# Performance work log

Hardware: AMD Instinct MI355X
Metric: run time of the kernel (lower is better)

Reference implementation:

```python
import jax, jax.numpy as jnp
import numpy as np

B, H, L, E = 32, 8, 512, 3
N_VARS = 8
TOP_P = 0.5
NOISE_EPS = 0.01
EPS = 1e-10


def setup_inputs() -> dict:
    key = jax.random.key(0)
    k1, k2, k3 = jax.random.split(key, 3)
    scale = 1.0 / np.sqrt(L)  # sane logits for softmax
    x = jax.random.normal(k1, (B, H, L, L), dtype=jnp.float32)
    gate_w = jax.random.normal(k2, (E, L), dtype=jnp.float32) * scale
    noise_w = jax.random.normal(k3, (E, L), dtype=jnp.float32) * scale
    return {"x": x, "gate_w": gate_w, "noise_w": noise_w}


def _build_masks(L, n_vars):
    # Vectorized version of the torch per-k loop building [L, 3, L] masks.
    N = L // n_vars
    j = jnp.arange(L)          # target position
    k = jnp.arange(L)[:, None]  # source position
    S = ((j % N == k % N) & (j != k)).astype(jnp.float32)   # same offset, different var
    T = ((j // N) == (k // N)).astype(jnp.float32)           # same variable block
    ST = 1.0 - S - T
    return jnp.stack([S, T, ST], axis=1)  # [L, 3, L]


def _noisy_top_p_gating(xf, gate_w, noise_w, key):
    # xf: [BH, L, L] -> logits [BH, L, E]
    clean_logits = jnp.einsum('ble,ne->bln', xf, gate_w)
    noise_stddev = jax.nn.softplus(jnp.einsum('ble,ne->bln', xf, noise_w)) + NOISE_EPS
    noisy_logits = clean_logits + jax.random.normal(key, clean_logits.shape, clean_logits.dtype) * noise_stddev
    probs = jax.nn.softmax(noisy_logits, axis=-1)  # softmax over experts (dim 2)
    # dynamic (entropy) loss: sum over L dim (dim=1), mean over rest
    loss_dynamic = -(probs * jnp.log(probs + EPS)).sum(axis=1).mean()
    # sort descending over experts
    order = jnp.argsort(-probs, axis=-1)
    sorted_probs = jnp.take_along_axis(probs, order, axis=-1)
    cum = jnp.cumsum(sorted_probs, axis=-1)
    mask = cum > TOP_P
    # keep the first expert that crosses the threshold
    thr_idx = jnp.argmax(mask.astype(jnp.int32), axis=-1)          # [BH, L]
    thr_mask = jnp.arange(E) == thr_idx[..., None]                 # one-hot bool
    mask = mask & ~thr_mask
    # scatter kept (mask==0) sorted positions back to original expert ids:
    # top_p_mask[..., sorted_indices[..., k]] = (mask[..., k] == 0)
    inv = jnp.argsort(order, axis=-1)
    top_p_mask = jnp.take_along_axis((~mask).astype(jnp.float32), inv, axis=-1)
    # importance loss on masked sorted probs summed over batch dim
    kept = jnp.where(mask, 0.0, sorted_probs)
    importance = kept.sum(axis=0)  # [L, E]
    loss_importance = jnp.var(importance, ddof=1) / (importance.mean() ** 2 + EPS)
    loss = loss_importance + 0.1 * loss_dynamic
    return top_p_mask, loss


def reference(x, gate_w, noise_w):
    Bx, Hx, Lx, _ = x.shape
    xf = x.reshape(Bx * Hx, Lx, Lx)
    gates, loss = _noisy_top_p_gating(xf, gate_w, noise_w, jax.random.key(42))
    gates = gates.reshape(Bx, Hx, Lx, E).astype(jnp.float32)
    masks = _build_masks(Lx, N_VARS)            # [L, 3, L]
    mask_base = jnp.eye(Lx, dtype=jnp.float32)[None, None]
    out = jnp.einsum('bhli,lid->bhld', gates, masks) + mask_base
    return (out, loss)
```

## Files before the change

kernel.cpp:

```cpp
#include <hip/hip_runtime.h>
#include <cstdint>
#include <cstddef>


namespace {

constexpr int kBH = 256;
constexpr int kL = 512;
constexpr int kE = 3;
constexpr int kRows = kBH * kL;

typedef float v4f __attribute__((ext_vector_type(4)));

__device__ __forceinline__ uint32_t rotl32(uint32_t v, int n) {
  return (v << n) | (v >> (32 - n));
}

__device__ __forceinline__ void threefry2x32_k42(uint32_t& x0, uint32_t& x1) {
  const uint32_t ks0 = 0u;
  const uint32_t ks1 = 42u;
  const uint32_t ks2 = 0u ^ 42u ^ 0x1BD11BDAu;
  x0 += ks0; x1 += ks1;
#define TF_ROUND(r) { x0 += x1; x1 = rotl32(x1, (r)); x1 ^= x0; }
  TF_ROUND(13) TF_ROUND(15) TF_ROUND(26) TF_ROUND(6)
  x0 += ks1; x1 += ks2 + 1u;
  TF_ROUND(17) TF_ROUND(29) TF_ROUND(16) TF_ROUND(24)
  x0 += ks2; x1 += ks0 + 2u;
  TF_ROUND(13) TF_ROUND(15) TF_ROUND(26) TF_ROUND(6)
  x0 += ks0; x1 += ks1 + 3u;
  TF_ROUND(17) TF_ROUND(29) TF_ROUND(16) TF_ROUND(24)
  x0 += ks1; x1 += ks2 + 4u;
  TF_ROUND(13) TF_ROUND(15) TF_ROUND(26) TF_ROUND(6)
  x0 += ks2; x1 += ks0 + 5u;
#undef TF_ROUND
}

__device__ __forceinline__ uint32_t jax_random_bits(uint32_t flat_idx) {
  uint32_t x0 = 0u;
  uint32_t x1 = flat_idx;
  threefry2x32_k42(x0, x1);
  return x0 ^ x1;
}

__device__ float bits_to_normal(uint32_t bits) {
#pragma clang fp contract(off)
  const uint32_t fb = (bits >> 9) | 0x3F800000u;
  const float f = __uint_as_float(fb) - 1.0f;
  const float lo = -0.99999994f;
  float u = f * 2.0f + lo;
  u = fmaxf(lo, u);
  float w = -log1pf(-(u * u));
  float p;
  if (w < 5.0f) {
    w = w - 2.5f;
    p = 2.81022636e-08f;
    p = 3.43273939e-07f + p * w;
    p = -3.5233877e-06f + p * w;
    p = -4.39150654e-06f + p * w;
    p = 0.00021858087f + p * w;
    p = -0.00125372503f + p * w;
    p = -0.00417768164f + p * w;
    p = 0.246640727f + p * w;
    p = 1.50140941f + p * w;
  } else {
    w = sqrtf(w) - 3.0f;
    p = -0.000200214257f;
    p = 0.000100950558f + p * w;
    p = 0.00134934322f + p * w;
    p = -0.00367342844f + p * w;
    p = 0.00573950773f + p * w;
    p = -0.0076224613f + p * w;
    p = 0.00943887047f + p * w;
    p = 1.00167406f + p * w;
    p = 2.83297682f + p * w;
  }
  const float einv = p * u;
  return 1.41421354f * einv;
}

__device__ __forceinline__ float softplus_f32(float v) {
#pragma clang fp contract(off)
  const float amax = fmaxf(v, 0.0f);
  return amax + log1pf(expf(-fabsf(v)));
}

#define LOADG(BUF, OFF)                                                     \
  _Pragma("unroll")                                                         \
  for (int i_ = 0; i_ < 4; ++i_)                                            \
    BUF[i_] = *reinterpret_cast<const float4*>(xr + (OFF) + i_ * 4);

#define COMP16(BUF, KB)                                                     \
  {                                                                         \
    _Pragma("unroll")                                                       \
    for (int j_ = 0; j_ < 4; ++j_) {                                        \
      const int k_ = (KB) + j_ * 4;                                         \
      const float4 wg0 = *reinterpret_cast<const float4*>(gw + k_);         \
      const float4 wg1 = *reinterpret_cast<const float4*>(gw + kL + k_);    \
      const float4 wg2 = *reinterpret_cast<const float4*>(gw + 2*kL + k_);  \
      const float4 wn0 = *reinterpret_cast<const float4*>(nw + k_);         \
      const float4 wn1 = *reinterpret_cast<const float4*>(nw + kL + k_);    \
      const float4 wn2 = *reinterpret_cast<const float4*>(nw + 2*kL + k_);  \
      const float4 xq = BUF[j_];                                            \
      accg[0] = fmaf(xq.x, wg0.x, accg[0]);                                 \
      accg[1] = fmaf(xq.x, wg1.x, accg[1]);                                 \
      accg[2] = fmaf(xq.x, wg2.x, accg[2]);                                 \
      accn[0] = fmaf(xq.x, wn0.x, accn[0]);                                 \
      accn[1] = fmaf(xq.x, wn1.x, accn[1]);                                 \
      accn[2] = fmaf(xq.x, wn2.x, accn[2]);                                 \
      accg[0] = fmaf(xq.y, wg0.y, accg[0]);                                 \
      accg[1] = fmaf(xq.y, wg1.y, accg[1]);                                 \
      accg[2] = fmaf(xq.y, wg2.y, accg[2]);                                 \
      accn[0] = fmaf(xq.y, wn0.y, accn[0]);                                 \
      accn[1] = fmaf(xq.y, wn1.y, accn[1]);                                 \
      accn[2] = fmaf(xq.y, wn2.y, accn[2]);                                 \
      accg[0] = fmaf(xq.z, wg0.z, accg[0]);                                 \
      accg[1] = fmaf(xq.z, wg1.z, accg[1]);                                 \
      accg[2] = fmaf(xq.z, wg2.z, accg[2]);                                 \
      accn[0] = fmaf(xq.z, wn0.z, accn[0]);                                 \
      accn[1] = fmaf(xq.z, wn1.z, accn[1]);                                 \
      accn[2] = fmaf(xq.z, wn2.z, accn[2]);                                 \
      accg[0] = fmaf(xq.w, wg0.w, accg[0]);                                 \
      accg[1] = fmaf(xq.w, wg1.w, accg[1]);                                 \
      accg[2] = fmaf(xq.w, wg2.w, accg[2]);                                 \
      accn[0] = fmaf(xq.w, wn0.w, accn[0]);                                 \
      accn[1] = fmaf(xq.w, wn1.w, accn[1]);                                 \
      accn[2] = fmaf(xq.w, wn2.w, accn[2]);                                 \
    }                                                                       \
  }

__global__ __launch_bounds__(256) void gating_kernel(
    const float* __restrict__ x, const float* __restrict__ gw,
    const float* __restrict__ nw, float* __restrict__ g_out,
    float* __restrict__ kept_out, float* __restrict__ ent_out) {
  const int t = threadIdx.x;
  const int r = blockIdx.x * 256 + t;
  const float* xr = x + (size_t)r * kL;

  float accg[3] = {0.f, 0.f, 0.f};
  float accn[3] = {0.f, 0.f, 0.f};
  {
    float4 bufA[4], bufB[4];
    LOADG(bufA, 0)
    for (int k0 = 0; k0 < kL; k0 += 32) {
      LOADG(bufB, k0 + 16)
      COMP16(bufA, k0)
      if (k0 + 32 < kL) { LOADG(bufA, k0 + 32) }
      COMP16(bufB, k0 + 16)
    }
  }

  {
#pragma clang fp contract(off)
    float noisy[3];
    const uint32_t nbase = (uint32_t)r * 3u;
#pragma unroll
    for (int e = 0; e < 3; ++e) {
      const float cl = accg[e];
      const float sp = softplus_f32(accn[e]) + 0.01f;
      const float nz = bits_to_normal(jax_random_bits(nbase + (uint32_t)e));
      const float prod = nz * sp;
      noisy[e] = cl + prod;
    }
    const float m = fmaxf(noisy[0], fmaxf(noisy[1], noisy[2]));
    float uu[3];
    uu[0] = expf(noisy[0] - m);
    uu[1] = expf(noisy[1] - m);
    uu[2] = expf(noisy[2] - m);
    const float ssum = (uu[0] + uu[1]) + uu[2];
    float p[3];
    p[0] = uu[0] / ssum;
    p[1] = uu[1] / ssum;
    p[2] = uu[2] / ssum;

    int o0 = 0;
    if (p[1] > p[o0]) o0 = 1;
    if (p[2] > p[o0]) o0 = 2;
    const int i = (o0 == 0) ? 1 : 0;
    const int j = (o0 == 2) ? 1 : 2;
    const int o1 = (p[j] > p[i]) ? j : i;

    const float s0 = p[o0];
    const float s1 = p[o1];
    const bool keep2 = !(s0 > 0.5f);

    float g[3] = {0.f, 0.f, 0.f};
    g[o0] = 1.f;
    if (keep2) g[o1] = 1.f;

    float ent = 0.f;
    ent += p[0] * logf(p[0] + 1e-10f);
    ent += p[1] * logf(p[1] + 1e-10f);
    ent += p[2] * logf(p[2] + 1e-10f);

    const int bh = r >> 9;
    const int l = r & (kL - 1);
    g_out[r * 3 + 0] = g[0];
    g_out[r * 3 + 1] = g[1];
    g_out[r * 3 + 2] = g[2];
    kept_out[(0 * kL + l) * kBH + bh] = s0;
    kept_out[(1 * kL + l) * kBH + bh] = keep2 ? s1 : 0.f;
    kept_out[(2 * kL + l) * kBH + bh] = 0.f;
    ent_out[r] = -ent;
  }
}

__global__ __launch_bounds__(256) void loss_partial_kernel(
    const float* __restrict__ kept, const float* __restrict__ ent,
    double* __restrict__ imp_ws, double* __restrict__ ent_ws) {
  __shared__ double red[256];
  const int t = threadIdx.x;
  const int ln = t & 63;
  const int wg = blockIdx.x * 4 + (t >> 6);

#pragma unroll
  for (int rep = 0; rep < 3; ++rep) {
    const int q = wg + rep * 512;
    const float4 v = reinterpret_cast<const float4*>(kept + (size_t)q * kBH)[ln];
    double s = ((double)v.x + (double)v.y) + ((double)v.z + (double)v.w);
#pragma unroll
    for (int off = 32; off > 0; off >>= 1) s += __shfl_xor(s, off, 64);
    if (ln == 0) imp_ws[q] = s;
  }

  double a = 0.0;
#pragma unroll
  for (int it = 0; it < 4; ++it) {
    a += (double)ent[blockIdx.x * 1024 + it * 256 + t];
  }
  red[t] = a;
  __syncthreads();
  for (int off = 128; off > 0; off >>= 1) {
    if (t < off) red[t] += red[t + off];
    __syncthreads();
  }
  if (t == 0) ent_ws[blockIdx.x] = red[0];
}

__global__ __launch_bounds__(256) void out_kernel(
    const float* __restrict__ g, const double* __restrict__ imp_ws,
    const double* __restrict__ ent_ws, float* __restrict__ out,
    float* __restrict__ loss_out) {
  const int td = threadIdx.x;

  if (blockIdx.x == 0) {
    __shared__ double red[256];
    __shared__ double s_mean;
    double a = 0.0;
    for (int i = td; i < kL * kE; i += 256) a += imp_ws[i];
    red[td] = a;
    __syncthreads();
    for (int off = 128; off > 0; off >>= 1) {
      if (td < off) red[td] += red[td + off];
      __syncthreads();
    }
    if (td == 0) s_mean = red[0] / (double)(kL * kE);
    __syncthreads();
    const double mean = s_mean;

    double sq = 0.0;
    for (int i = td; i < kL * kE; i += 256) {
      const double d = imp_ws[i] - mean;
      sq += d * d;
    }
    red[td] = sq;
    __syncthreads();
    for (int off = 128; off > 0; off >>= 1) {
      if (td < off) red[td] += red[td + off];
      __syncthreads();
    }
    const double var_sum = red[0];
    __syncthreads();

    double e = 0.0;
    for (int i = td; i < 128; i += 256) e += ent_ws[i];
    red[td] = e;
    __syncthreads();
    for (int off = 128; off > 0; off >>= 1) {
      if (td < off) red[td] += red[td + off];
      __syncthreads();
    }
    if (td == 0) {
      const double var = var_sum / (double)(kL * kE - 1);
      const double loss_imp = var / (mean * mean + 1e-10);
      const double loss_dyn = red[0] / 768.0;
      loss_out[0] = (float)(loss_imp + 0.1 * loss_dyn);
    }
  }

  const int r = blockIdx.x * 8 + (td >> 5);
  const int l = r & (kL - 1);
  const float g0 = g[r * 3 + 0];
  const float g1 = g[r * 3 + 1];
  const float g2 = g[r * 3 + 2];
  const int lblk = l >> 6;
  const int loff = l & 63;
  float* orow = out + (size_t)r * kL;
  const int c0 = (td & 31) * 4;
#pragma unroll
  for (int j = 0; j < 4; ++j) {
    const int d0 = c0 + j * 128;
    v4f vals;
#pragma unroll
    for (int k = 0; k < 4; ++k) {
      const int d = d0 + k;
      float v;
      if (((d & 63) == loff) && (d != l)) v = g0;
      else if ((d >> 6) == lblk) v = g1;
      else v = g2;
      if (d == l) v += 1.0f;
      vals[k] = v;
    }
    __builtin_nontemporal_store(vals, reinterpret_cast<v4f*>(orow + d0));
  }
}

}

extern "C" void kernel_launch(void* const* d_in, const int* in_sizes, int n_in,
                              void* d_out, int out_size, void* d_ws, size_t ws_size,
                              hipStream_t stream) {
  (void)in_sizes; (void)n_in; (void)out_size; (void)ws_size;
  const float* x = (const float*)d_in[0];
  const float* gw = (const float*)d_in[1];
  const float* nw = (const float*)d_in[2];
  float* out = (float*)d_out;

  float* ws = (float*)d_ws;
  float* ws_g = ws;
  float* ws_kept = ws + (size_t)kRows * 3;
  float* ws_ent = ws + (size_t)kRows * 6;
  double* ws_imp = (double*)(ws + (size_t)kRows * 7);
  double* ws_entp = ws_imp + kL * kE;

  gating_kernel<<<kRows / 256, 256, 0, stream>>>(x, gw, nw, ws_g, ws_kept, ws_ent);
  loss_partial_kernel<<<128, 256, 0, stream>>>(ws_kept, ws_ent, ws_imp, ws_entp);
  out_kernel<<<kRows / 8, 256, 0, stream>>>(ws_g, ws_imp, ws_entp, out,
                                            out + (size_t)kBH * kL * kL);
}
```

Baseline: 124.5 us.

## Stage x tiles through padded double-buffered LDS for coalesced global loads

Before this change each thread streamed its own 2 KB row of x directly from global memory, so neighbouring lanes touched addresses 2 KB apart and loads were poorly coalesced. Now the block cooperatively loads 32-column tiles of its 256 rows with coalesced float4 reads, writes them into a padded, double-buffered shared-memory array, and each thread reads its row back from LDS. The next tile's global load is issued before computing on the current one. The cost is about 72 KB of LDS per block, which may limit occupancy, plus a barrier per tile.

New measurement: 114.8 us (median of 2 runs). 1.08x faster.

```diff
diff --git a/kernel.cpp b/kernel.cpp
--- a/kernel.cpp
+++ b/kernel.cpp
@@ -9,6 +9,7 @@
 constexpr int kL = 512;
 constexpr int kE = 3;
 constexpr int kRows = kBH * kL;
+constexpr int kPad = 36;
 
 typedef float v4f __attribute__((ext_vector_type(4)));
 
@@ -83,11 +84,6 @@
   const float amax = fmaxf(v, 0.0f);
   return amax + log1pf(expf(-fabsf(v)));
 }
-
-#define LOADG(BUF, OFF)                                                     \
-  _Pragma("unroll")                                                         \
-  for (int i_ = 0; i_ < 4; ++i_)                                            \
-    BUF[i_] = *reinterpret_cast<const float4*>(xr + (OFF) + i_ * 4);
 
 #define COMP16(BUF, KB)                                                     \
   {                                                                         \
@@ -128,25 +124,64 @@
     }                                                                       \
   }
 
+#define STAGE_LOAD(ST, K0)                                                  \
+  _Pragma("unroll")                                                         \
+  for (int i_ = 0; i_ < 8; ++i_) {                                          \
+    const int fi_ = i_ * 256 + t;                                           \
+    const int row_ = fi_ >> 3;                                              \
+    const int c4_ = fi_ & 7;                                                \
+    ST[i_] = *reinterpret_cast<const float4*>(                              \
+        xblk + (size_t)row_ * kL + (K0) + c4_ * 4);                         \
+  }
+
+#define STAGE_WRITE(ST, BUF)                                                \
+  _Pragma("unroll")                                                         \
+  for (int i_ = 0; i_ < 8; ++i_) {                                          \
+    const int fi_ = i_ * 256 + t;                                           \
+    const int row_ = fi_ >> 3;                                              \
+    const int c4_ = fi_ & 7;                                                \
+    *reinterpret_cast<float4*>(&s_x[BUF][row_ * kPad + c4_ * 4]) = ST[i_];  \
+  }
+
 __global__ __launch_bounds__(256) void gating_kernel(
     const float* __restrict__ x, const float* __restrict__ gw,
     const float* __restrict__ nw, float* __restrict__ g_out,
     float* __restrict__ kept_out, float* __restrict__ ent_out) {
+  __shared__ float s_x[2][256 * kPad];
   const int t = threadIdx.x;
   const int r = blockIdx.x * 256 + t;
-  const float* xr = x + (size_t)r * kL;
+  const float* xblk = x + (size_t)blockIdx.x * 256 * kL;
+
+  {
+    float4 st[8];
+    STAGE_LOAD(st, 0)
+    STAGE_WRITE(st, 0)
+  }
+  __syncthreads();
 
   float accg[3] = {0.f, 0.f, 0.f};
   float accn[3] = {0.f, 0.f, 0.f};
-  {
-    float4 bufA[4], bufB[4];
-    LOADG(bufA, 0)
-    for (int k0 = 0; k0 < kL; k0 += 32) {
-      LOADG(bufB, k0 + 16)
-      COMP16(bufA, k0)
-      if (k0 + 32 < kL) { LOADG(bufA, k0 + 32) }
-      COMP16(bufB, k0 + 16)
-    }
+  for (int tile = 0; tile < 16; ++tile) {
+    const int k0 = tile * 32;
+    float4 st[8];
+    if (tile < 15) { STAGE_LOAD(st, k0 + 32) }
+    {
+#pragma clang fp contract(off)
+      const float* xrow = &s_x[tile & 1][t * kPad];
+      float4 bufL[4];
+      bufL[0] = *reinterpret_cast<const float4*>(xrow);
+      bufL[1] = *reinterpret_cast<const float4*>(xrow + 4);
+      bufL[2] = *reinterpret_cast<const float4*>(xrow + 8);
+      bufL[3] = *reinterpret_cast<const float4*>(xrow + 12);
+      COMP16(bufL, k0)
+      bufL[0] = *reinterpret_cast<const float4*>(xrow + 16);
+      bufL[1] = *reinterpret_cast<const float4*>(xrow + 20);
+      bufL[2] = *reinterpret_cast<const float4*>(xrow + 24);
+      bufL[3] = *reinterpret_cast<const float4*>(xrow + 28);
+      COMP16(bufL, k0 + 16)
+    }
+    if (tile < 15) { STAGE_WRITE(st, (tile + 1) & 1) }
+    __syncthreads();
   }
 
   {
```

## Stage x tiles through LDS via async global_load_lds with XOR swizzle

Applied to the files above, without the earlier changes.

Replaces per-thread strided float4 global loads of each row with cooperative global_load_lds transfers into a double-buffered 64 KB shared tile. Each wave loads 8-row by 32-column chunks so global reads are coalesced across rows, and an XOR swizzle on the 16-byte column index is meant to avoid LDS bank conflicts when each thread reads back its own row. The intent is better memory coalescing for a bandwidth-bound GEMV-like reduction. In exchange it adds a block-wide barrier per tile and heavy LDS use, which lowers occupancy.

Measured after the change: 132.7 us. 6.6% more time.

```diff
diff --git a/kernel.cpp b/kernel.cpp
--- a/kernel.cpp
+++ b/kernel.cpp
@@ -11,6 +11,11 @@
 constexpr int kRows = kBH * kL;
 
 typedef float v4f __attribute__((ext_vector_type(4)));
+
+#define GLOAD_LDS16(GP, LP)                                                 \
+  __builtin_amdgcn_global_load_lds(                                         \
+      (const __attribute__((address_space(1))) uint32_t*)(GP),              \
+      (__attribute__((address_space(3))) uint32_t*)(LP), 16, 0, 0)
 
 __device__ __forceinline__ uint32_t rotl32(uint32_t v, int n) {
   return (v << n) | (v >> (32 - n));
@@ -83,11 +88,6 @@
   const float amax = fmaxf(v, 0.0f);
   return amax + log1pf(expf(-fabsf(v)));
 }
-
-#define LOADG(BUF, OFF)                                                     \
-  _Pragma("unroll")                                                         \
-  for (int i_ = 0; i_ < 4; ++i_)                                            \
-    BUF[i_] = *reinterpret_cast<const float4*>(xr + (OFF) + i_ * 4);
 
 #define COMP16(BUF, KB)                                                     \
   {                                                                         \
@@ -132,21 +132,48 @@
     const float* __restrict__ x, const float* __restrict__ gw,
     const float* __restrict__ nw, float* __restrict__ g_out,
     float* __restrict__ kept_out, float* __restrict__ ent_out) {
+  __shared__ float s_x[2][256 * 32];
   const int t = threadIdx.x;
+  const int ln = t & 63;
+  const int wv = t >> 6;
   const int r = blockIdx.x * 256 + t;
-  const float* xr = x + (size_t)r * kL;
+  const float* xblk = x + (size_t)blockIdx.x * 256 * kL;
+  const int rowin = ln >> 3;
+  const int srcc4 = ((ln & 7) ^ rowin) * 4;
+
+#define STAGE_GL(K0, BUF)                                                   \
+  _Pragma("unroll")                                                         \
+  for (int i_ = 0; i_ < 8; ++i_) {                                          \
+    const int c_ = wv * 8 + i_;                                             \
+    GLOAD_LDS16(xblk + (size_t)(c_ * 8 + rowin) * kL + (K0) + srcc4,        \
+                &s_x[BUF][c_ * 256]);                                       \
+  }
+
+  STAGE_GL(0, 0)
+  __syncthreads();
 
   float accg[3] = {0.f, 0.f, 0.f};
   float accn[3] = {0.f, 0.f, 0.f};
-  {
-    float4 bufA[4], bufB[4];
-    LOADG(bufA, 0)
-    for (int k0 = 0; k0 < kL; k0 += 32) {
-      LOADG(bufB, k0 + 16)
-      COMP16(bufA, k0)
-      if (k0 + 32 < kL) { LOADG(bufA, k0 + 32) }
-      COMP16(bufB, k0 + 16)
-    }
+  const int sw = t & 7;
+  for (int tile = 0; tile < 16; ++tile) {
+    const int k0 = tile * 32;
+    if (tile < 15) { STAGE_GL(k0 + 32, (tile + 1) & 1) }
+    {
+#pragma clang fp contract(off)
+      const float* xrow = &s_x[tile & 1][t * 32];
+      float4 bufL[4];
+      bufL[0] = *reinterpret_cast<const float4*>(xrow + ((0 ^ sw) << 2));
+      bufL[1] = *reinterpret_cast<const float4*>(xrow + ((1 ^ sw) << 2));
+      bufL[2] = *reinterpret_cast<const float4*>(xrow + ((2 ^ sw) << 2));
+      bufL[3] = *reinterpret_cast<const float4*>(xrow + ((3 ^ sw) << 2));
+      COMP16(bufL, k0)
+      bufL[0] = *reinterpret_cast<const float4*>(xrow + ((4 ^ sw) << 2));
+      bufL[1] = *reinterpret_cast<const float4*>(xrow + ((5 ^ sw) << 2));
+      bufL[2] = *reinterpret_cast<const float4*>(xrow + ((6 ^ sw) << 2));
+      bufL[3] = *reinterpret_cast<const float4*>(xrow + ((7 ^ sw) << 2));
+      COMP16(bufL, k0 + 16)
+    }
+    __syncthreads();
   }
 
   {
```
